# Kernel tuning notes

Hardware: AMD Instinct MI355X
Metric: run time of the kernel (lower is better)

## Reference

```python
import jax, jax.numpy as jnp
import numpy as np

D = 1024
H = 16
HD = D // H
R = 16
EPS = 1e-5


def _ln(x, w, b):
    mu = jnp.mean(x, axis=-1, keepdims=True)
    var = jnp.mean((x - mu) ** 2, axis=-1, keepdims=True)
    return (x - mu) * jax.lax.rsqrt(var + EPS) * w + b


def setup_inputs() -> dict:
    key = jax.random.key(0)
    ks = jax.random.split(key, 8)
    B, N = 32, 257
    s = 0.02
    return {
        "q_x": jax.random.normal(ks[0], (B, N, D), jnp.float32),
        "ln1_w": jnp.ones((D,), jnp.float32),
        "ln1_b": jnp.zeros((D,), jnp.float32),
        "in_proj_w": jax.random.normal(ks[1], (3 * D, D), jnp.float32) * s,
        "in_proj_b": jnp.zeros((3 * D,), jnp.float32),
        "out_w": jax.random.normal(ks[2], (D, D), jnp.float32) * s,
        "out_b": jnp.zeros((D,), jnp.float32),
        "ln2_w": jnp.ones((D,), jnp.float32),
        "ln2_b": jnp.zeros((D,), jnp.float32),
        "fc_w": jax.random.normal(ks[3], (4 * D, D), jnp.float32) * s,
        "fc_b": jnp.zeros((4 * D,), jnp.float32),
        "proj_w": jax.random.normal(ks[4], (D, 4 * D), jnp.float32) * s,
        "proj_b": jnp.zeros((D,), jnp.float32),
    }


def reference(q_x, ln1_w, ln1_b, in_proj_w, in_proj_b, out_w, out_b,
              ln2_w, ln2_b, fc_w, fc_b, proj_w, proj_b):
    B, N, _ = q_x.shape
    # --- attention (no size bias / no padding mask on first call) ---
    h = _ln(q_x, ln1_w, ln1_b)
    qkv = h @ in_proj_w.T + in_proj_b            # [B,N,3D]
    q, k, v = jnp.split(qkv, 3, axis=-1)
    to_heads = lambda t: t.reshape(B, N, H, HD).transpose(0, 2, 1, 3)  # [B,H,N,hd]
    q, k, v = to_heads(q), to_heads(k), to_heads(v)
    metric = k.mean(axis=1)                      # [B,N,hd] ToMe metric
    attn = jax.nn.softmax(jnp.einsum('bhnd,bhmd->bhnm', q, k) / np.sqrt(HD).astype(np.float32), axis=-1)
    o = jnp.einsum('bhnm,bhmd->bhnd', attn, v).transpose(0, 2, 1, 3).reshape(B, N, D)
    x = q_x + (o @ out_w.T + out_b)
    # --- ToMe: bipartite soft matching + weighted-average merge (size=None -> ones) ---
    r = min(R, (N - 1) // 2)                     # class token protected
    m = metric / jnp.linalg.norm(metric, axis=-1, keepdims=True)
    a, bm = m[:, ::2, :], m[:, 1::2, :]          # [B,Na,hd], [B,Nb,hd]
    scores = jnp.einsum('bnd,bmd->bnm', a, bm)
    scores = scores.at[:, 0, :].set(-jnp.inf)    # never merge class token
    node_max = scores.max(axis=-1)               # [B,Na]
    node_idx = scores.argmax(axis=-1)            # [B,Na]
    edge_idx = jnp.argsort(-node_max, axis=-1)   # descending similarity
    unm_idx = jnp.sort(edge_idx[:, r:], axis=-1) # keep order; cls token first
    src_idx = edge_idx[:, :r]
    dst_idx = jnp.take_along_axis(node_idx, src_idx, axis=1)  # [B,r]
    bi = jnp.arange(B)[:, None]

    def merge_sum(t):
        s, d = t[:, ::2], t[:, 1::2]
        unm = jnp.take_along_axis(s, unm_idx[:, :, None], axis=1)
        src = jnp.take_along_axis(s, src_idx[:, :, None], axis=1)
        d = d.at[bi, dst_idx].add(src)
        return jnp.concatenate([unm, d], axis=1)  # [B, N-r, C]

    size = jnp.ones((B, N, 1), x.dtype)
    x = merge_sum(x * size)
    size = merge_sum(size)
    x = x / size
    # --- MLP ---
    h2 = _ln(x, ln2_w, ln2_b)
    h2 = jax.nn.gelu(h2 @ fc_w.T + fc_b, approximate=False)
    x = x + (h2 @ proj_w.T + proj_b)
    return x
```

## Files before the change

kernel.cpp:

```cpp
#include <hip/hip_runtime.h>
#include <math.h>

#define D_ 1024
#define H_ 16
#define HD_ 64
#define BATCH 32
#define NTOK 257
#define NROWS (BATCH*NTOK)
#define NE 129
#define NO 128
#define RR 16
#define UNM 113
#define NMERGED 241
#define MROWS (BATCH*NMERGED)
#define SELSTRIDE 288

typedef unsigned short u16;
typedef unsigned int u32;
typedef __bf16 bf16x8 __attribute__((ext_vector_type(8)));
typedef float floatx4 __attribute__((ext_vector_type(4)));

__device__ __forceinline__ u16 f2bf(float f) {
    u32 u = __float_as_uint(f);
    u += 0x7fffu + ((u >> 16) & 1u);
    return (u16)(u >> 16);
}
__device__ __forceinline__ float bflo(u32 v) { return __uint_as_float(v << 16); }
__device__ __forceinline__ float bfhi(u32 v) { return __uint_as_float(v & 0xffff0000u); }

__global__ __launch_bounds__(256) void ln_kernel(const float* __restrict__ x,
                                                 const float* __restrict__ w,
                                                 const float* __restrict__ bia,
                                                 float* __restrict__ outf,
                                                 u16* __restrict__ outb) {
    int row = blockIdx.x;
    const float* xr = x + (size_t)row * D_;
    int t = threadIdx.x;
    float v[4];
#pragma unroll
    for (int i = 0; i < 4; i++) v[i] = xr[t + 256 * i];
    float s = v[0] + v[1] + v[2] + v[3];
#pragma unroll
    for (int o = 32; o; o >>= 1) s += __shfl_down(s, o);
    __shared__ float sm[8];
    int wv = t >> 6, ln = t & 63;
    if (ln == 0) sm[wv] = s;
    __syncthreads();
    float mu = (sm[0] + sm[1] + sm[2] + sm[3]) * (1.0f / D_);
    float d0 = v[0] - mu, d1 = v[1] - mu, d2 = v[2] - mu, d3 = v[3] - mu;
    float q = d0 * d0 + d1 * d1 + d2 * d2 + d3 * d3;
#pragma unroll
    for (int o = 32; o; o >>= 1) q += __shfl_down(q, o);
    if (ln == 0) sm[4 + wv] = q;
    __syncthreads();
    float var = (sm[4] + sm[5] + sm[6] + sm[7]) * (1.0f / D_);
    float rs = rsqrtf(var + 1e-5f);
#pragma unroll
    for (int i = 0; i < 4; i++) {
        int c = t + 256 * i;
        float o = (v[i] - mu) * rs * w[c] + bia[c];
        if (outf) outf[(size_t)row * D_ + c] = o;
        if (outb) outb[(size_t)row * D_ + c] = f2bf(o);
    }
}

__global__ __launch_bounds__(256) void wm_kernel(const float* __restrict__ W,
                                                 const float* __restrict__ bias,
                                                 float* __restrict__ WmT,
                                                 float* __restrict__ bm) {
    int e = blockIdx.x * 256 + threadIdx.x;
    if (e < 64 * 1024) {
        int d = e >> 10, c = e & 1023;
        float s = 0.f;
#pragma unroll
        for (int hh = 0; hh < 16; hh++)
            s += W[(size_t)(1024 + hh * 64 + d) * 1024 + c];
        WmT[(size_t)c * 64 + d] = s * (1.0f / 16.0f);
    }
    if (e < 64) {
        float s = 0.f;
        for (int hh = 0; hh < 16; hh++) s += bias[1024 + hh * 64 + e];
        bm[e] = s * (1.0f / 16.0f);
    }
}

__global__ __launch_bounds__(256) void castw_kernel(const float* __restrict__ s0,
                                                    const float* __restrict__ s1,
                                                    const float* __restrict__ s2,
                                                    const float* __restrict__ s3,
                                                    u16* __restrict__ d0, u16* __restrict__ d1,
                                                    u16* __restrict__ d2, u16* __restrict__ d3) {
    size_t gi = ((size_t)blockIdx.x * 256 + threadIdx.x) * 8;
    const float* s; u16* d; size_t off;
    if (gi < 3145728)        { s = s0; d = d0; off = gi; }
    else if (gi < 4194304)   { s = s1; d = d1; off = gi - 3145728; }
    else if (gi < 8388608)   { s = s2; d = d2; off = gi - 4194304; }
    else                     { s = s3; d = d3; off = gi - 8388608; }
    float4 a = *(const float4*)(s + off);
    float4 b = *(const float4*)(s + off + 4);
    uint4 o;
    o.x = (u32)f2bf(a.x) | ((u32)f2bf(a.y) << 16);
    o.y = (u32)f2bf(a.z) | ((u32)f2bf(a.w) << 16);
    o.z = (u32)f2bf(b.x) | ((u32)f2bf(b.y) << 16);
    o.w = (u32)f2bf(b.z) | ((u32)f2bf(b.w) << 16);
    *(uint4*)(d + off) = o;
}

__global__ __launch_bounds__(256) void metric_kernel(const float* __restrict__ A,
                                                     const float* __restrict__ WmT,
                                                     const float* __restrict__ bm,
                                                     float* __restrict__ metric) {
    int wv = threadIdx.x >> 6, ln = threadIdx.x & 63;
    int row0 = blockIdx.x * 16 + wv * 4;
    const float* a0 = A + (size_t)row0 * 1024;
    float acc0 = 0.f, acc1 = 0.f, acc2 = 0.f, acc3 = 0.f;
    for (int k = 0; k < 1024; k += 8) {
#pragma unroll
        for (int kk = 0; kk < 8; kk++) {
            float w = WmT[(size_t)(k + kk) * 64 + ln];
            acc0 = fmaf(a0[k + kk], w, acc0);
            acc1 = fmaf(a0[1024 + k + kk], w, acc1);
            acc2 = fmaf(a0[2048 + k + kk], w, acc2);
            acc3 = fmaf(a0[3072 + k + kk], w, acc3);
        }
    }
    float b = bm[ln];
    metric[(size_t)row0 * 64 + ln] = acc0 + b;
    metric[(size_t)(row0 + 1) * 64 + ln] = acc1 + b;
    metric[(size_t)(row0 + 2) * 64 + ln] = acc2 + b;
    metric[(size_t)(row0 + 3) * 64 + ln] = acc3 + b;
}

__global__ __launch_bounds__(256) void mgemm_kernel(const u16* __restrict__ A,
                                                    const u16* __restrict__ Bw,
                                                    const float* __restrict__ bias,
                                                    const float* __restrict__ resid,
                                                    void* __restrict__ Cv,
                                                    int M, int N, int K, int mode) {
    __shared__ u16 As[128 * 64];
    __shared__ u16 Bs[128 * 64];
    int tid = threadIdx.x;
    int wv = tid >> 6, ln = tid & 63;
    int m0 = blockIdx.y * 128, n0 = blockIdx.x * 128;
    int sr = wv * 8 + (ln >> 3);
    int sc = ((ln & 7) ^ (ln >> 3)) * 8;
    const u16* Ag[4]; const u16* Bg[4];
#pragma unroll
    for (int i = 0; i < 4; i++) {
        Ag[i] = A + (size_t)(m0 + i * 32 + sr) * K + sc;
        Bg[i] = Bw + (size_t)(n0 + i * 32 + sr) * K + sc;
    }
    floatx4 acc[4][4];
#pragma unroll
    for (int i = 0; i < 4; i++)
#pragma unroll
        for (int j = 0; j < 4; j++) acc[i][j] = (floatx4){0.f, 0.f, 0.f, 0.f};
    int wm = (wv & 1) * 64, wn = (wv >> 1) * 64;
    int lane16 = ln & 15, lq = ln >> 4;
    int sw = lane16 & 7;

    for (int k0 = 0; k0 < K; k0 += 64) {
        __syncthreads();
#pragma unroll
        for (int i = 0; i < 4; i++) {
            __builtin_amdgcn_global_load_lds(
                (const __attribute__((address_space(1))) void*)(Ag[i] + k0),
                (__attribute__((address_space(3))) void*)&As[i * 2048 + wv * 512], 16, 0, 0);
            __builtin_amdgcn_global_load_lds(
                (const __attribute__((address_space(1))) void*)(Bg[i] + k0),
                (__attribute__((address_space(3))) void*)&Bs[i * 2048 + wv * 512], 16, 0, 0);
        }
        __syncthreads();
#pragma unroll
        for (int ks = 0; ks < 2; ks++) {
            bf16x8 af[4], bf[4];
#pragma unroll
            for (int t = 0; t < 4; t++) {
                int slot = ((ks * 4 + lq) ^ sw) * 8;
                af[t] = *(const bf16x8*)&As[(wm + t * 16 + lane16) * 64 + slot];
                bf[t] = *(const bf16x8*)&Bs[(wn + t * 16 + lane16) * 64 + slot];
            }
#pragma unroll
            for (int mt = 0; mt < 4; mt++)
#pragma unroll
                for (int nt = 0; nt < 4; nt++)
                    acc[mt][nt] = __builtin_amdgcn_mfma_f32_16x16x32_bf16(
                        af[mt], bf[nt], acc[mt][nt], 0, 0, 0);
        }
    }
#pragma unroll
    for (int mt = 0; mt < 4; mt++) {
#pragma unroll
        for (int nt = 0; nt < 4; nt++) {
            int col = n0 + wn + nt * 16 + lane16;
            float bv = bias[col];
#pragma unroll
            for (int r = 0; r < 4; r++) {
                int row = m0 + wm + mt * 16 + lq * 4 + r;
                if (row < M) {
                    float v = acc[mt][nt][r] + bv;
                    if (mode == 1) {
                        ((float*)Cv)[(size_t)row * N + col] = v + resid[(size_t)row * N + col];
                    } else {
                        if (mode == 2) v = 0.5f * v * (1.0f + erff(v * 0.70710678118654752f));
                        ((u16*)Cv)[(size_t)row * N + col] = f2bf(v);
                    }
                }
            }
        }
    }
}

#define VST 296
#define PST 40
__global__ __launch_bounds__(256, 3) void fattn_kernel(const u16* __restrict__ qkv,
                                                       u16* __restrict__ o) {
    __shared__ __align__(16) u16 Vts[64 * VST];
    __shared__ __align__(16) u16 Pb[4][16 * PST];
    int b = blockIdx.x / H_, h = blockIdx.x % H_;
    int tid = threadIdx.x;
    int wv = tid >> 6, ln = tid & 63;
    int lane16 = ln & 15, lq = ln >> 4;
    const u16* base = qkv + (size_t)b * NTOK * 3072 + h * HD_;

    for (int idx = tid; idx < NTOK * 8; idx += 256) {
        int key = idx >> 3, d0 = (idx & 7) * 8;
        uint4 u = *(const uint4*)(base + (size_t)key * 3072 + 2048 + d0);
        u16 e[8] = {(u16)u.x, (u16)(u.x >> 16), (u16)u.y, (u16)(u.y >> 16),
                    (u16)u.z, (u16)(u.z >> 16), (u16)u.w, (u16)(u.w >> 16)};
#pragma unroll
        for (int i = 0; i < 8; i++) Vts[(d0 + i) * VST + key] = e[i];
    }
    for (int idx = tid; idx < 64 * 32; idx += 256) {
        int d = idx >> 5, c = idx & 31;
        if (c) Vts[d * VST + 256 + c] = 0;
    }
    __syncthreads();

    u16* Pw = &Pb[wv][0];
    for (int qt = wv; qt < 17; qt += 4) {
        int q0 = qt * 16;
        const u16* qp = base + (size_t)(q0 + lane16) * 3072 + lq * 8;
        bf16x8 af0 = *(const bf16x8*)(qp);
        bf16x8 af1 = *(const bf16x8*)(qp + 32);
        floatx4 accs[17];
#pragma unroll
        for (int nt = 0; nt < 17; nt++) {
            const u16* kp = base + (size_t)(nt * 16 + lane16) * 3072 + 1024 + lq * 8;
            bf16x8 kb0 = *(const bf16x8*)(kp);
            bf16x8 kb1 = *(const bf16x8*)(kp + 32);
            floatx4 z = (floatx4){0.f, 0.f, 0.f, 0.f};
            z = __builtin_amdgcn_mfma_f32_16x16x32_bf16(af0, kb0, z, 0, 0, 0);
            accs[nt] = __builtin_amdgcn_mfma_f32_16x16x32_bf16(af1, kb1, z, 0, 0, 0);
        }
        if (lane16 != 0) {
#pragma unroll
            for (int r = 0; r < 4; r++) accs[16][r] = -3.0e38f;
        }
        float mrow[4], lsum[4], inv[4];
#pragma unroll
        for (int r = 0; r < 4; r++) {
            float m = -3.0e38f;
#pragma unroll
            for (int nt = 0; nt < 17; nt++) m = fmaxf(m, accs[nt][r]);
#pragma unroll
            for (int off = 1; off < 16; off <<= 1) m = fmaxf(m, __shfl_xor(m, off));
            mrow[r] = m;
            lsum[r] = 0.f;
        }
#pragma unroll
        for (int nt = 0; nt < 17; nt++) {
#pragma unroll
            for (int r = 0; r < 4; r++) {
                float p = __expf((accs[nt][r] - mrow[r]) * 0.125f);
                accs[nt][r] = p;
                lsum[r] += p;
            }
        }
#pragma unroll
        for (int r = 0; r < 4; r++) {
#pragma unroll
            for (int off = 1; off < 16; off <<= 1) lsum[r] += __shfl_xor(lsum[r], off);
            inv[r] = 1.0f / lsum[r];
        }
        floatx4 acco[4];
#pragma unroll
        for (int dt = 0; dt < 4; dt++) acco[dt] = (floatx4){0.f, 0.f, 0.f, 0.f};
#pragma unroll
        for (int ks = 0; ks < 9; ks++) {
            int nt0 = 2 * ks, nt1 = 2 * ks + 1;
#pragma unroll
            for (int r = 0; r < 4; r++) {
                float p0 = accs[nt0][r];
                float p1 = (nt1 <= 16) ? accs[nt1][r] : 0.f;
                Pw[(lq * 4 + r) * PST + lane16] = f2bf(p0);
                Pw[(lq * 4 + r) * PST + 16 + lane16] = f2bf(p1);
            }
            bf16x8 pa = *(const bf16x8*)&Pw[lane16 * PST + lq * 8];
#pragma unroll
            for (int dt = 0; dt < 4; dt++) {
                bf16x8 vb = *(const bf16x8*)&Vts[(dt * 16 + lane16) * VST + ks * 32 + lq * 8];
                acco[dt] = __builtin_amdgcn_mfma_f32_16x16x32_bf16(pa, vb, acco[dt], 0, 0, 0);
            }
        }
#pragma unroll
        for (int dt = 0; dt < 4; dt++) {
#pragma unroll
            for (int r = 0; r < 4; r++) {
                int row = q0 + lq * 4 + r;
                if (row < NTOK)
                    o[((size_t)(b * NTOK + row)) * D_ + h * HD_ + dt * 16 + lane16] =
                        f2bf(acco[dt][r] * inv[r]);
            }
        }
    }
}

__global__ __launch_bounds__(256) void tome_select_kernel(const float* __restrict__ metric,
                                                          int* __restrict__ sel) {
    __shared__ float bm[NO * HD_];
    __shared__ float nmax[NE];
    __shared__ int nidx[NE];
    int b = blockIdx.x, tid = threadIdx.x;
    const float* mb = metric + (size_t)b * NTOK * HD_;
    if (tid < NO) {
        const float* r = mb + (size_t)(2 * tid + 1) * HD_;
        float ss = 0.f;
#pragma unroll
        for (int c = 0; c < HD_; c++) ss += r[c] * r[c];
        float inv = rsqrtf(ss);
        for (int c = 0; c < HD_; c++) bm[tid * HD_ + c] = r[c] * inv;
    }
    __syncthreads();
    if (tid < NE) {
        float best = -3.0e38f; int bi = 0;
        if (tid != 0) {
            const float* r = mb + (size_t)(2 * tid) * HD_;
            float ss = 0.f;
#pragma unroll
            for (int c = 0; c < HD_; c++) ss += r[c] * r[c];
            float inv = rsqrtf(ss);
            float a[HD_];
#pragma unroll
            for (int c = 0; c < HD_; c++) a[c] = r[c] * inv;
            for (int j = 0; j < NO; j++) {
                float s = 0.f;
#pragma unroll
                for (int c = 0; c < HD_; c++) s = fmaf(a[c], bm[j * HD_ + c], s);
                if (s > best) { best = s; bi = j; }
            }
        }
        nmax[tid] = best; nidx[tid] = bi;
    }
    __syncthreads();
    if (tid == 0) {
        int* sb = sel + b * SELSTRIDE;
        int* src = sb;
        int* dst = sb + 16;
        int* cnt = sb + 32;
        int* unm = sb + 160;
        bool used[NE];
        for (int i = 0; i < NE; i++) used[i] = false;
        for (int j = 0; j < NO; j++) cnt[j] = 0;
        for (int s = 0; s < RR; s++) {
            float bv = -3.0e38f; int bi = 0;
            for (int i = 0; i < NE; i++)
                if (!used[i] && nmax[i] > bv) { bv = nmax[i]; bi = i; }
            used[bi] = true;
            src[s] = bi;
            int d2 = nidx[bi];
            dst[s] = d2;
            cnt[d2]++;
        }
        int u = 0;
        for (int i = 0; i < NE; i++) if (!used[i]) unm[u++] = i;
    }
}

__global__ __launch_bounds__(256) void merge_kernel(const float* __restrict__ x,
                                                    const int* __restrict__ sel,
                                                    float* __restrict__ xm) {
    int blk = blockIdx.x;
    int b = blk / NMERGED, t = blk % NMERGED;
    const int* sb = sel + b * SELSTRIDE;
    int tid = threadIdx.x;
    const float* xb = x + (size_t)b * NTOK * D_;
    float* orow = xm + ((size_t)b * NMERGED + t) * D_;
    if (t < UNM) {
        int srcRow = 2 * sb[160 + t];
        const float* r = xb + (size_t)srcRow * D_;
#pragma unroll
        for (int i = 0; i < 4; i++) orow[tid + 256 * i] = r[tid + 256 * i];
    } else {
        int j = t - UNM;
        const float* r = xb + (size_t)(2 * j + 1) * D_;
        float v[4];
#pragma unroll
        for (int i = 0; i < 4; i++) v[i] = r[tid + 256 * i];
        int c = sb[32 + j];
        if (c > 0) {
            for (int s = 0; s < RR; s++) {
                if (sb[16 + s] == j) {
                    const float* rs = xb + (size_t)(2 * sb[s]) * D_;
#pragma unroll
                    for (int i = 0; i < 4; i++) v[i] += rs[tid + 256 * i];
                }
            }
            float inv = 1.0f / (float)(1 + c);
#pragma unroll
            for (int i = 0; i < 4; i++) v[i] *= inv;
        }
#pragma unroll
        for (int i = 0; i < 4; i++) orow[tid + 256 * i] = v[i];
    }
}

extern "C" void kernel_launch(void* const* d_in, const int* in_sizes, int n_in,
                              void* d_out, int out_size, void* d_ws, size_t ws_size,
                              hipStream_t stream) {
    (void)in_sizes; (void)n_in; (void)out_size; (void)ws_size;
    const float* qx   = (const float*)d_in[0];
    const float* ln1w = (const float*)d_in[1];
    const float* ln1b = (const float*)d_in[2];
    const float* ipw  = (const float*)d_in[3];
    const float* ipb  = (const float*)d_in[4];
    const float* outw = (const float*)d_in[5];
    const float* outb = (const float*)d_in[6];
    const float* ln2w = (const float*)d_in[7];
    const float* ln2b = (const float*)d_in[8];
    const float* fcw  = (const float*)d_in[9];
    const float* fcb  = (const float*)d_in[10];
    const float* pw   = (const float*)d_in[11];
    const float* pb   = (const float*)d_in[12];
    float* out = (float*)d_out;

    char* ws = (char*)d_ws;
    u16*   qkvb  = (u16*)(ws + 0);
    u16*   h2b   = (u16*)(ws + 0);
    u16*   hb    = (u16*)(ws + 51118080);
    float* hf    = (float*)(ws + 68157440);
    float* xbuf  = hf;
    u16*   ob    = (u16*)(ws + 101842944);
    float* metric= (float*)(ws + 118882304);
    float* xm    = (float*)(ws + 120987648);
    u16*   ln2bb = (u16*)(ws + 152576000);
    u16*   wqkv  = (u16*)(ws + 168566784);
    u16*   woutb = (u16*)(ws + 174858240);
    u16*   wfc   = (u16*)(ws + 176955392);
    u16*   wproj = (u16*)(ws + 185344000);
    float* WmT   = (float*)(ws + 193732608);
    float* bm    = (float*)(ws + 193994752);
    int*   sel   = (int*)(ws + 193995008);

    ln_kernel<<<NROWS, 256, 0, stream>>>(qx, ln1w, ln1b, hf, hb);
    wm_kernel<<<256, 256, 0, stream>>>(ipw, ipb, WmT, bm);
    castw_kernel<<<6144, 256, 0, stream>>>(ipw, outw, fcw, pw, wqkv, woutb, wfc, wproj);
    metric_kernel<<<514, 256, 0, stream>>>(hf, WmT, bm, metric);
    mgemm_kernel<<<dim3(24, 65), 256, 0, stream>>>(hb, wqkv, ipb, nullptr, qkvb,
                                                   NROWS, 3072, 1024, 0);
    fattn_kernel<<<BATCH * H_, 256, 0, stream>>>(qkvb, ob);
    mgemm_kernel<<<dim3(8, 65), 256, 0, stream>>>(ob, woutb, outb, qx, xbuf,
                                                  NROWS, 1024, 1024, 1);
    tome_select_kernel<<<BATCH, 256, 0, stream>>>(metric, sel);
    merge_kernel<<<BATCH * NMERGED, 256, 0, stream>>>(xbuf, sel, xm);
    ln_kernel<<<MROWS, 256, 0, stream>>>(xm, ln2w, ln2b, nullptr, ln2bb);
    mgemm_kernel<<<dim3(32, 61), 256, 0, stream>>>(ln2bb, wfc, fcb, nullptr, h2b,
                                                   MROWS, 4096, 1024, 2);
    mgemm_kernel<<<dim3(8, 61), 256, 0, stream>>>(h2b, wproj, pb, xm, out,
                                                  MROWS, 1024, 4096, 1);
}
```

Measured before the change: 906.3 us.

## Split ToMe selection into parallel normalize, score, and wave-level pick kernels

Replaces the single per-batch ToMe selection kernel, which ran 32 blocks with per-thread serial dot products and a single-thread top-r loop, with three kernels. The first normalizes metric rows with wave reductions and writes a transposed B matrix. The second computes scores with one wave per A node and reduces with shuffles to get the argmax. The third does the r greedy picks with wave shuffles instead of a serial scan. The goal is to remove a latency-bound serial stage, at the cost of two extra launches and some intermediate buffers.

```diff
diff --git a/kernel.cpp b/kernel.cpp
--- a/kernel.cpp
+++ b/kernel.cpp
@@ -25,8 +25,6 @@
     u += 0x7fffu + ((u >> 16) & 1u);
     return (u16)(u >> 16);
 }
-__device__ __forceinline__ float bflo(u32 v) { return __uint_as_float(v << 16); }
-__device__ __forceinline__ float bfhi(u32 v) { return __uint_as_float(v & 0xffff0000u); }
 
 __global__ __launch_bounds__(256) void ln_kernel(const float* __restrict__ x,
                                                  const float* __restrict__ w,
@@ -316,65 +314,92 @@
     }
 }
 
-__global__ __launch_bounds__(256) void tome_select_kernel(const float* __restrict__ metric,
-                                                          int* __restrict__ sel) {
-    __shared__ float bm[NO * HD_];
-    __shared__ float nmax[NE];
-    __shared__ int nidx[NE];
-    int b = blockIdx.x, tid = threadIdx.x;
-    const float* mb = metric + (size_t)b * NTOK * HD_;
-    if (tid < NO) {
-        const float* r = mb + (size_t)(2 * tid + 1) * HD_;
-        float ss = 0.f;
-#pragma unroll
-        for (int c = 0; c < HD_; c++) ss += r[c] * r[c];
-        float inv = rsqrtf(ss);
-        for (int c = 0; c < HD_; c++) bm[tid * HD_ + c] = r[c] * inv;
-    }
+__global__ __launch_bounds__(256) void mnorm_kernel(const float* __restrict__ metric,
+                                                    float* __restrict__ aN,
+                                                    float* __restrict__ bT) {
+    int r = blockIdx.x * 4 + (threadIdx.x >> 6);
+    int l = threadIdx.x & 63;
+    int b = r / NTOK, t = r % NTOK;
+    float v = metric[(size_t)r * 64 + l];
+    float ss = v * v;
+#pragma unroll
+    for (int off = 1; off < 64; off <<= 1) ss += __shfl_xor(ss, off);
+    float nv = v * rsqrtf(ss);
+    if (!(t & 1)) aN[((size_t)b * NE + (t >> 1)) * 64 + l] = nv;
+    else          bT[(size_t)b * 8192 + l * 128 + (t >> 1)] = nv;
+}
+
+__global__ __launch_bounds__(256) void score_kernel(const float* __restrict__ aN,
+                                                    const float* __restrict__ bT,
+                                                    float* __restrict__ nodeMax,
+                                                    int* __restrict__ nodeIdx) {
+    __shared__ float aL[4][64];
+    int b = blockIdx.x / 33, eb = blockIdx.x % 33;
+    int wv = threadIdx.x >> 6, l = threadIdx.x & 63;
+    int e = eb * 4 + wv;
+    if (e >= NE) return;
+    aL[wv][l] = aN[((size_t)b * NE + e) * 64 + l];
+    const float* bp = bT + (size_t)b * 8192;
+    float s0 = 0.f, s1 = 0.f;
+#pragma unroll 8
+    for (int c = 0; c < 64; c++) {
+        float w = aL[wv][c];
+        s0 = fmaf(w, bp[c * 128 + l], s0);
+        s1 = fmaf(w, bp[c * 128 + 64 + l], s1);
+    }
+    float bv; int bj;
+    if (s1 > s0) { bv = s1; bj = l + 64; } else { bv = s0; bj = l; }
+    if (e == 0) { bv = -3.0e38f; bj = 0; }
+#pragma unroll
+    for (int off = 1; off < 64; off <<= 1) {
+        float ov = __shfl_xor(bv, off);
+        int oj = __shfl_xor(bj, off);
+        if (ov > bv || (ov == bv && oj < bj)) { bv = ov; bj = oj; }
+    }
+    if (l == 0) { nodeMax[b * NE + e] = bv; nodeIdx[b * NE + e] = bj; }
+}
+
+__global__ __launch_bounds__(64) void pick_kernel(const float* __restrict__ nodeMax,
+                                                  const int* __restrict__ nodeIdx,
+                                                  int* __restrict__ sel) {
+    __shared__ unsigned char usedL[NE];
+    __shared__ int cntL[NO];
+    int b = blockIdx.x, l = threadIdx.x;
+    int* sb = sel + b * SELSTRIDE;
+    float v0 = nodeMax[b * NE + l];
+    float v1 = nodeMax[b * NE + 64 + l];
+    float v2 = (l == 0) ? nodeMax[b * NE + 128] : -3.0e38f;
+    u32 usedM = (l == 0) ? 0u : 4u;
+    cntL[l] = 0; cntL[l + 64] = 0;
+    for (int s = 0; s < RR; s++) {
+        float bv = -3.0e38f; int be = 1 << 30;
+        if (!(usedM & 1u) && v0 > bv) { bv = v0; be = l; }
+        if (!(usedM & 2u) && v1 > bv) { bv = v1; be = l + 64; }
+        if (!(usedM & 4u) && v2 > bv) { bv = v2; be = l + 128; }
+#pragma unroll
+        for (int off = 1; off < 64; off <<= 1) {
+            float ov = __shfl_xor(bv, off);
+            int oe = __shfl_xor(be, off);
+            if (ov > bv || (ov == bv && oe < be)) { bv = ov; be = oe; }
+        }
+        if ((be & 63) == l) usedM |= 1u << (be >> 6);
+        if (l == 0) {
+            sb[s] = be;
+            int d = nodeIdx[b * NE + be];
+            sb[16 + s] = d;
+            cntL[d]++;
+        }
+    }
+    usedL[l] = (usedM & 1u) ? 1 : 0;
+    usedL[64 + l] = (usedM & 2u) ? 1 : 0;
+    if (l == 0) usedL[128] = (usedM & 4u) ? 1 : 0;
     __syncthreads();
-    if (tid < NE) {
-        float best = -3.0e38f; int bi = 0;
-        if (tid != 0) {
-            const float* r = mb + (size_t)(2 * tid) * HD_;
-            float ss = 0.f;
-#pragma unroll
-            for (int c = 0; c < HD_; c++) ss += r[c] * r[c];
-            float inv = rsqrtf(ss);
-            float a[HD_];
-#pragma unroll
-            for (int c = 0; c < HD_; c++) a[c] = r[c] * inv;
-            for (int j = 0; j < NO; j++) {
-                float s = 0.f;
-#pragma unroll
-                for (int c = 0; c < HD_; c++) s = fmaf(a[c], bm[j * HD_ + c], s);
-                if (s > best) { best = s; bi = j; }
-            }
-        }
-        nmax[tid] = best; nidx[tid] = bi;
-    }
-    __syncthreads();
-    if (tid == 0) {
-        int* sb = sel + b * SELSTRIDE;
-        int* src = sb;
-        int* dst = sb + 16;
-        int* cnt = sb + 32;
-        int* unm = sb + 160;
-        bool used[NE];
-        for (int i = 0; i < NE; i++) used[i] = false;
-        for (int j = 0; j < NO; j++) cnt[j] = 0;
-        for (int s = 0; s < RR; s++) {
-            float bv = -3.0e38f; int bi = 0;
-            for (int i = 0; i < NE; i++)
-                if (!used[i] && nmax[i] > bv) { bv = nmax[i]; bi = i; }
-            used[bi] = true;
-            src[s] = bi;
-            int d2 = nidx[bi];
-            dst[s] = d2;
-            cnt[d2]++;
-        }
+    if (l == 0) {
         int u = 0;
-        for (int i = 0; i < NE; i++) if (!used[i]) unm[u++] = i;
-    }
+        for (int e = 0; e < NE; e++) if (!usedL[e]) sb[160 + u++] = e;
+    }
+    sb[32 + l] = cntL[l];
+    sb[32 + 64 + l] = cntL[l + 64];
 }
 
 __global__ __launch_bounds__(256) void merge_kernel(const float* __restrict__ x,
@@ -451,6 +476,10 @@
     float* WmT   = (float*)(ws + 193732608);
     float* bm    = (float*)(ws + 193994752);
     int*   sel   = (int*)(ws + 193995008);
+    float* aN    = (float*)(ws + 194031872);
+    float* bT    = (float*)(ws + 195088640);
+    float* nMax  = (float*)(ws + 196137216);
+    int*   nIdx  = (int*)(ws + 196153856);
 
     ln_kernel<<<NROWS, 256, 0, stream>>>(qx, ln1w, ln1b, hf, hb);
     wm_kernel<<<256, 256, 0, stream>>>(ipw, ipb, WmT, bm);
@@ -461,7 +490,9 @@
     fattn_kernel<<<BATCH * H_, 256, 0, stream>>>(qkvb, ob);
     mgemm_kernel<<<dim3(8, 65), 256, 0, stream>>>(ob, woutb, outb, qx, xbuf,
                                                   NROWS, 1024, 1024, 1);
-    tome_select_kernel<<<BATCH, 256, 0, stream>>>(metric, sel);
+    mnorm_kernel<<<2056, 256, 0, stream>>>(metric, aN, bT);
+    score_kernel<<<BATCH * 33, 256, 0, stream>>>(aN, bT, nMax, nIdx);
+    pick_kernel<<<BATCH, 64, 0, stream>>>(nMax, nIdx, sel);
     merge_kernel<<<BATCH * NMERGED, 256, 0, stream>>>(xbuf, sel, xm);
     ln_kernel<<<MROWS, 256, 0, stream>>>(xm, ln2w, ln2b, nullptr, ln2bb);
     mgemm_kernel<<<dim3(32, 61), 256, 0, stream>>>(ln2bb, wfc, fcb, nullptr, h2b,
```

After: 792.8 us. 12.5% less time.
